# Kernel optimization log

Hardware: AMD Instinct MI355X
Metric: run time of the kernel (lower is better)

Reference implementation:

```python
import jax, jax.numpy as jnp
import numpy as np

NUM_SEM, MAXPP, FS, FG, H, ITERS, ETN, GROUPS = 24, 10, 128, 128, 128, 2, 4, 16
N_NODES, N_EDGES = 20000, 320000


def _leaky(x):
    return jax.nn.leaky_relu(x, 0.01)


def _lin_init(k, din, dout):
    kw, kb = jax.random.split(k)
    lim = 1.0 / np.sqrt(din)
    w = jax.random.uniform(kw, (dout, din), jnp.float32, -lim, lim)
    b = jax.random.uniform(kb, (dout,), jnp.float32, -lim, lim)
    return w, b


def setup_inputs() -> dict:
    key = jax.random.key(0)
    ks = jax.random.split(key, 16)
    inp = {}
    inp["child_feats"] = jax.random.normal(ks[0], (1, N_NODES, NUM_SEM + MAXPP + FS), jnp.float32)
    inp["child_geo_feats"] = jax.random.normal(ks[1], (1, N_NODES, FG), jnp.float32)
    inp["child_exists"] = jnp.ones((1, N_NODES, 1), jnp.float32)
    inp["edge_type_onehot"] = jax.random.uniform(ks[2], (1, N_EDGES, ETN), jnp.float32)
    inp["edge_indices"] = jax.random.randint(ks[3], (1, N_EDGES, 2), 0, N_NODES)
    inp["child_op_w"], inp["child_op_b"] = _lin_init(ks[4], NUM_SEM + MAXPP + FS, H)
    inp["second_w"], inp["second_b"] = _lin_init(ks[5], H * (ITERS + 1), FS)
    ew, eb = zip(*[_lin_init(ks[6 + i], 2 * H + ETN, H) for i in range(ITERS)])
    inp["edge_w"] = jnp.stack(ew)
    inp["edge_b"] = jnp.stack(eb)
    inp["child_geo_w"], inp["child_geo_b"] = _lin_init(ks[10], FG, H)
    inp["second_geo_w"], inp["second_geo_b"] = _lin_init(ks[11], H, FG)
    inp["gn_w"] = jnp.ones((FG,), jnp.float32)
    inp["gn_b"] = jnp.zeros((FG,), jnp.float32)
    inp["skip_w"], inp["skip_b"] = _lin_init(ks[12], FG, FG)
    return inp


def _group_norm(x, w, b, groups=GROUPS, eps=1e-5):
    # x: [B, C]  (torch GroupNorm on 2D input)
    B, C = x.shape
    xg = x.reshape(B, groups, C // groups)
    mu = xg.mean(axis=-1, keepdims=True)
    var = xg.var(axis=-1, keepdims=True)
    xn = ((xg - mu) * jax.lax.rsqrt(var + eps)).reshape(B, C)
    return xn * w + b


def reference(child_feats, child_geo_feats, child_exists, edge_type_onehot, edge_indices,
              child_op_w, child_op_b, second_w, second_b, edge_w, edge_b,
              child_geo_w, child_geo_b, second_geo_w, second_geo_b, gn_w, gn_b, skip_w, skip_b):
    B, N, _ = child_feats.shape
    # struct branch
    cf = (child_feats @ child_op_w.T + child_op_b) * child_exists  # [B,N,H]
    iter_parent_feats = [cf.max(axis=1)]                           # symmetric_type='max'
    idx_from = edge_indices[0, :, 0]
    idx_to = edge_indices[0, :, 1]
    ef = edge_type_onehot[0]                                       # [E,ETN]
    for i in range(ITERS):
        # gather endpoints, concat edge type, edge-MLP + leaky relu
        msg = jnp.concatenate([cf[0, idx_from], cf[0, idx_to], ef], axis=1)  # [E,2H+ETN]
        msg = _leaky(msg @ edge_w[i].T + edge_b[i])                          # [E,H]
        # scatter_max into zero-initialized node slots (matches torch_scatter with out=zeros)
        cf = jnp.zeros((N, H), msg.dtype).at[idx_from].max(msg)[None]        # [1,N,H]
        iter_parent_feats.append(cf.max(axis=1))
    parent_feat = _leaky(jnp.concatenate(iter_parent_feats, axis=1) @ second_w.T + second_b)
    # geo branch
    skip = (child_geo_feats @ skip_w.T + skip_b) * child_exists    # [B,N,FG]
    cg = (child_geo_feats @ child_geo_w.T + child_geo_b) * child_exists  # [B,N,H]
    pg = _leaky(cg.max(axis=1))
    sg = _leaky(skip.max(axis=1))
    parent_geo_feat = _leaky(sg + _group_norm(pg @ second_geo_w.T + second_geo_b, gn_w, gn_b))
    return parent_feat, parent_geo_feat
```

## Files before the change

kernel.cpp:

```cpp
#include <hip/hip_runtime.h>

#define N_NODES 20000
#define N_EDGES 320000
#define HD 128
#define FIN 162
#define KE 260
#define KPAD 288
#define KOP 192
#define WSTR 296
#define OSTR 200
#define GSTR 136
#define TSTR 136
#define RSTR 260

typedef unsigned short u16;
typedef __attribute__((ext_vector_type(8))) short bf16x8;
typedef __attribute__((ext_vector_type(4))) float f32x4;

__device__ __forceinline__ float leaky(float x){ return fmaxf(x, 0.01f*x); }
__device__ __forceinline__ unsigned fmap(float f){
    unsigned u = __float_as_uint(f);
    return (u & 0x80000000u) ? ~u : (u | 0x80000000u);
}
__device__ __forceinline__ float funmap(unsigned u){
    return __uint_as_float((u & 0x80000000u) ? (u & 0x7fffffffu) : ~u);
}
__device__ __forceinline__ unsigned umax_(unsigned a, unsigned b){ return a > b ? a : b; }
__device__ __forceinline__ u16 f2bf(float x){
    unsigned b = __float_as_uint(x);
    return (u16)((b + 0x7fffu + ((b >> 16) & 1u)) >> 16);
}
__device__ __forceinline__ float bf2f(u16 u){
    return __uint_as_float(((unsigned)u) << 16);
}
__device__ __forceinline__ unsigned cvt_pk_bf16(float lo, float hi){
    unsigned r;
    asm("v_cvt_pk_bf16_f32 %0, %1, %2" : "=v"(r) : "v"(lo), "v"(hi));
    return r;
}

#define PB_W 16
#define PB_F 960
#define PB_G 640
#define PB_H 320
#define PREP_GRID (PB_W + PB_F + PB_G + PB_H)

__global__ __launch_bounds__(256) void prep(
    const float* __restrict__ edge_w, const float* __restrict__ edge_bias,
    u16* __restrict__ Wb,
    const float* __restrict__ op_w,   u16* __restrict__ Wop,
    const float* __restrict__ geo_w,  u16* __restrict__ Wgeo,
    const float* __restrict__ skip_w, u16* __restrict__ Wskip,
    const float* __restrict__ feats,  u16* __restrict__ featsb,
    const float* __restrict__ geof,   u16* __restrict__ geob,
    const int* __restrict__ eidx, int* __restrict__ count)
{
    const int b = blockIdx.x, t = threadIdx.x;
    if (b < PB_W) {
        for (int idx = b * 256 + t; idx < 16384; idx += PB_W * 256) {
            union { u16 us[8]; uint4 v; } pk;
            if (idx < 9216) {
                int layer = idx / 4608, rem = idx - layer * 4608;
                int h = rem / 36, j = rem - h * 36;
                const float* src = edge_w + (size_t)layer * 128 * KE + h * KE;
                #pragma unroll
                for (int kk = 0; kk < 8; ++kk) {
                    int k = j * 8 + kk;
                    pk.us[kk] = (k < KE) ? f2bf(src[k])
                              : (k == 260) ? f2bf(edge_bias[layer * 128 + h])
                              : (u16)0;
                }
                ((uint4*)Wb)[(size_t)layer * 128 * 36 + h * 36 + j] = pk.v;
            } else if (idx < 12288) {
                int rem = idx - 9216;
                int h = rem / 24, j = rem - h * 24;
                const float* src = op_w + h * FIN;
                #pragma unroll
                for (int kk = 0; kk < 8; ++kk) {
                    int k = j * 8 + kk;
                    pk.us[kk] = (k < FIN) ? f2bf(src[k]) : (u16)0;
                }
                ((uint4*)Wop)[h * 24 + j] = pk.v;
            } else {
                int rem = idx - 12288;
                int which = rem >> 11;
                int r2 = rem & 2047;
                const float4* src = (const float4*)((which ? skip_w : geo_w)) + r2 * 2;
                float4 a = src[0], c = src[1];
                pk.us[0]=f2bf(a.x); pk.us[1]=f2bf(a.y); pk.us[2]=f2bf(a.z); pk.us[3]=f2bf(a.w);
                pk.us[4]=f2bf(c.x); pk.us[5]=f2bf(c.y); pk.us[6]=f2bf(c.z); pk.us[7]=f2bf(c.w);
                ((uint4*)(which ? Wskip : Wgeo))[r2] = pk.v;
            }
        }
    } else if (b < PB_W + PB_F) {
        for (int f = (b - PB_W) * 256 + t; f < N_NODES * 24; f += PB_F * 256) {
            int n = f / 24, j = f - n * 24;
            union { u16 us[8]; uint4 v; } pk;
            if (j < 20) {
                const float2* src = (const float2*)(feats + (size_t)n * FIN + j * 8);
                float2 p0 = src[0], p1 = src[1], p2 = src[2], p3 = src[3];
                pk.us[0]=f2bf(p0.x); pk.us[1]=f2bf(p0.y); pk.us[2]=f2bf(p1.x); pk.us[3]=f2bf(p1.y);
                pk.us[4]=f2bf(p2.x); pk.us[5]=f2bf(p2.y); pk.us[6]=f2bf(p3.x); pk.us[7]=f2bf(p3.y);
            } else if (j == 20) {
                float2 p = *(const float2*)(feats + (size_t)n * FIN + 160);
                pk.us[0]=f2bf(p.x); pk.us[1]=f2bf(p.y);
                pk.us[2]=pk.us[3]=pk.us[4]=pk.us[5]=pk.us[6]=pk.us[7]=0;
            } else {
                #pragma unroll
                for (int kk = 0; kk < 8; ++kk) pk.us[kk] = 0;
            }
            ((uint4*)featsb)[(size_t)n * 24 + j] = pk.v;
        }
    } else if (b < PB_W + PB_F + PB_G) {
        for (int g = (b - PB_W - PB_F) * 256 + t; g < N_NODES * 16; g += PB_G * 256) {
            const float4* s = (const float4*)geof + (size_t)g * 2;
            float4 a = s[0], c = s[1];
            union { u16 us[8]; uint4 v; } pk;
            pk.us[0]=f2bf(a.x); pk.us[1]=f2bf(a.y); pk.us[2]=f2bf(a.z); pk.us[3]=f2bf(a.w);
            pk.us[4]=f2bf(c.x); pk.us[5]=f2bf(c.y); pk.us[6]=f2bf(c.z); pk.us[7]=f2bf(c.w);
            ((uint4*)geob)[g] = pk.v;
        }
    } else {
        for (int e = (b - PB_W - PB_F - PB_G) * 256 + t; e < N_EDGES; e += PB_H * 256)
            atomicAdd(&count[eidx[2 * e]], 1);
    }
}

__global__ __launch_bounds__(1024) void scan_offsets(
    const int* __restrict__ count, int* __restrict__ offset)
{
    __shared__ int part[1024];
    const int t = threadIdx.x;
    const int lo = t * 20;
    const int hi = min(lo + 20, N_NODES);
    int s = 0;
    for (int n = lo; n < hi; ++n) s += count[n];
    part[t] = s;
    __syncthreads();
    for (int d = 1; d < 1024; d <<= 1) {
        int v = (t >= d) ? part[t - d] : 0;
        __syncthreads();
        part[t] += v;
        __syncthreads();
    }
    int run = (t > 0) ? part[t - 1] : 0;
    for (int n = lo; n < hi; ++n) { offset[n] = run; run += count[n]; }
}

__global__ __launch_bounds__(256) void mid(
    const int* __restrict__ eidx, const float* __restrict__ ef,
    const int* __restrict__ offset, int* __restrict__ cursor,
    int* __restrict__ from_p, int* __restrict__ to_p, uint2* __restrict__ efb_p,
    const u16* __restrict__ featsb, const u16* __restrict__ geob,
    const float* __restrict__ exists,
    const u16* __restrict__ Wop, const float* __restrict__ op_b,
    const u16* __restrict__ Wgeo, const float* __restrict__ geo_b,
    const u16* __restrict__ Wskip, const float* __restrict__ skip_b,
    u16* __restrict__ cf_a,
    unsigned* __restrict__ ipf0_m, unsigned* __restrict__ pg_m,
    unsigned* __restrict__ sg_m)
{
    __shared__ __align__(16) u16 smem[128 * OSTR];
    __shared__ float ex_s[128];
    __shared__ unsigned colmax_s[128];

    const int blk = blockIdx.x, t = threadIdx.x;
    if (blk < 1250) {
        int e = blk * 256 + t;
        int2 p = ((const int2*)eidx)[e];
        int pos = offset[p.x] + atomicAdd(&cursor[p.x], 1);
        from_p[pos] = p.x; to_p[pos] = p.y;
        float4 e4 = ((const float4*)ef)[e];
        efb_p[pos] = make_uint2(
            (unsigned)f2bf(e4.x) | ((unsigned)f2bf(e4.y) << 16),
            (unsigned)f2bf(e4.z) | ((unsigned)f2bf(e4.w) << 16));
        return;
    }
    const int b = blk - 1250;
    const int mode = (b < 157) ? 0 : (b < 314) ? 1 : 2;
    const int bx = b - (mode == 0 ? 0 : mode == 1 ? 157 : 314);
    const int base = bx * 128;
    const int wave = t >> 6, l = t & 63;
    const int quad = l >> 4, lc = l & 15;
    const int R0 = (wave >> 1) * 64;
    const int C0 = (wave & 1) * 64;

    const u16* W = (mode == 0) ? Wop : (mode == 1) ? Wgeo : Wskip;
    const float* bias = (mode == 0) ? op_b : (mode == 1) ? geo_b : skip_b;
    unsigned* accout = (mode == 0) ? ipf0_m : (mode == 1) ? pg_m : sg_m;
    const int KW = (mode == 0) ? KOP : HD;
    const int SW = (mode == 0) ? OSTR : GSTR;
    const int NCH = (mode == 0) ? 6 : 4;
    const u16* A = (mode == 0) ? featsb : geob;

    {
        const int r = t >> 1, half = t & 1;
        const int nu4 = KW / 16;
        const uint4* src = (const uint4*)(W + (size_t)r * KW) + half * nu4;
        uint4* dst = (uint4*)(smem + r * SW) + half * nu4;
        for (int i = 0; i < nu4; ++i) dst[i] = src[i];
    }
    if (t < 128) {
        int n = base + t; if (n >= N_NODES) n = N_NODES - 1;
        ex_s[t] = exists[n];
        colmax_s[t] = 0u;
    }
    __syncthreads();

    f32x4 acc[4][4];
    #pragma unroll
    for (int i = 0; i < 4; ++i)
        #pragma unroll
        for (int j = 0; j < 4; ++j) acc[i][j] = (f32x4){0.f, 0.f, 0.f, 0.f};

    int nd[4];
    #pragma unroll
    for (int ti = 0; ti < 4; ++ti) {
        int n = base + R0 + ti * 16 + lc;
        nd[ti] = (n < N_NODES) ? n : N_NODES - 1;
    }

    for (int c = 0; c < NCH; ++c) {
        bf16x8 af[4], bfr[4];
        #pragma unroll
        for (int ti = 0; ti < 4; ++ti)
            af[ti] = *(const bf16x8*)(A + (size_t)nd[ti] * KW + c * 32 + quad * 8);
        #pragma unroll
        for (int tj = 0; tj < 4; ++tj)
            bfr[tj] = *(const bf16x8*)(smem + (C0 + tj * 16 + lc) * SW + c * 32 + quad * 8);
        #pragma unroll
        for (int ti = 0; ti < 4; ++ti)
            #pragma unroll
            for (int tj = 0; tj < 4; ++tj)
                acc[ti][tj] = __builtin_amdgcn_mfma_f32_16x16x32_bf16(
                    af[ti], bfr[tj], acc[ti][tj], 0, 0, 0);
    }

    #pragma unroll
    for (int tj = 0; tj < 4; ++tj) {
        const int col = C0 + tj * 16 + lc;
        const float bc = bias[col];
        unsigned mx = 0u;
        #pragma unroll
        for (int ti = 0; ti < 4; ++ti) {
            #pragma unroll
            for (int r = 0; r < 4; ++r) {
                int row = R0 + ti * 16 + quad * 4 + r;
                float x = (acc[ti][tj][r] + bc) * ex_s[row];
                acc[ti][tj][r] = x;
                mx = umax_(mx, fmap(x));
            }
        }
        atomicMax(&colmax_s[col], mx);
    }
    __syncthreads();
    if (t < 128) atomicMax(&accout[t], colmax_s[t]);

    if (mode == 0) {
        #pragma unroll
        for (int ti = 0; ti < 4; ++ti)
            #pragma unroll
            for (int tj = 0; tj < 4; ++tj) {
                const int col = C0 + tj * 16 + lc;
                #pragma unroll
                for (int r = 0; r < 4; ++r)
                    smem[(R0 + ti * 16 + quad * 4 + r) * TSTR + col] = f2bf(acc[ti][tj][r]);
            }
        __syncthreads();
        #pragma unroll
        for (int i = 0; i < 8; ++i) {
            int idx = t + i * 256;
            int row = idx >> 4, c16 = idx & 15;
            int n = base + row;
            if (n < N_NODES) {
                uint4 v = *(const uint4*)(smem + row * TSTR + c16 * 8);
                *(uint4*)(cf_a + (size_t)n * HD + c16 * 8) = v;
            }
        }
    }
}

template<int REDUCE>
__global__ __launch_bounds__(512, 2) void edge_mfma(
    const u16* __restrict__ cfb,
    const int* __restrict__ from_p,
    const int* __restrict__ to_p,
    const uint2* __restrict__ efb_p,
    const u16* __restrict__ Wb,
    const int* __restrict__ offs,
    const int* __restrict__ cnt,
    u16* __restrict__ cf_bb,
    float* __restrict__ cf_b32,
    int* __restrict__ ipf_out)
{
    __shared__ __align__(16) u16 smem[128 * WSTR];
    __shared__ int colmax_s[128];

    const int t    = threadIdx.x;
    const int base = blockIdx.x * 512;
    const int wave = t >> 6, l = t & 63;
    const int quad = l >> 4, lc = l & 15;
    const int R0 = wave * 64;

    for (int idx = t; idx < 128 * 36; idx += 512) {
        int r = idx / 36, j = idx - r * 36;
        ((uint4*)(smem + r * WSTR))[j] = ((const uint4*)(Wb + (size_t)r * KPAD))[j];
    }
    if (t < 128) colmax_s[t] = 0;

    int nf[4], nt[4]; uint2 efr[4];
    #pragma unroll
    for (int ti = 0; ti < 4; ++ti) {
        int e = base + R0 + ti * 16 + lc;
        nf[ti]  = from_p[e];
        nt[ti]  = to_p[e];
        efr[ti] = efb_p[e];
    }
    __syncthreads();

    f32x4 acc[4][8];
    #pragma unroll
    for (int i = 0; i < 4; ++i)
        #pragma unroll
        for (int j = 0; j < 8; ++j) acc[i][j] = (f32x4){0.f, 0.f, 0.f, 0.f};

    #pragma unroll
    for (int c = 0; c < 8; ++c) {
        bf16x8 af[4], bfr[8];
        #pragma unroll
        for (int ti = 0; ti < 4; ++ti) {
            int node = (c < 4) ? nf[ti] : nt[ti];
            af[ti] = *(const bf16x8*)(cfb + node * HD + (c & 3) * 32 + quad * 8);
        }
        #pragma unroll
        for (int tj = 0; tj < 8; ++tj)
            bfr[tj] = *(const bf16x8*)(smem + (tj * 16 + lc) * WSTR + c * 32 + quad * 8);
        #pragma unroll
        for (int ti = 0; ti < 4; ++ti)
            #pragma unroll
            for (int tj = 0; tj < 8; ++tj)
                acc[ti][tj] = __builtin_amdgcn_mfma_f32_16x16x32_bf16(
                    af[ti], bfr[tj], acc[ti][tj], 0, 0, 0);
    }
    {
        bf16x8 af[4], bfr[8];
        #pragma unroll
        for (int ti = 0; ti < 4; ++ti) {
            union { bf16x8 v; unsigned u[4]; } p;
            p.u[0] = efr[ti].x; p.u[1] = efr[ti].y;
            p.u[2] = 0x00003f80u;
            p.u[3] = 0u;
            union { bf16x8 v; unsigned u[4]; } z;
            z.u[0] = z.u[1] = z.u[2] = z.u[3] = 0u;
            af[ti] = (quad == 0) ? p.v : z.v;
        }
        #pragma unroll
        for (int tj = 0; tj < 8; ++tj)
            bfr[tj] = *(const bf16x8*)(smem + (tj * 16 + lc) * WSTR + 8 * 32 + quad * 8);
        #pragma unroll
        for (int ti = 0; ti < 4; ++ti)
            #pragma unroll
            for (int tj = 0; tj < 8; ++tj)
                acc[ti][tj] = __builtin_amdgcn_mfma_f32_16x16x32_bf16(
                    af[ti], bfr[tj], acc[ti][tj], 0, 0, 0);
    }

    #pragma unroll
    for (int tj = 0; tj < 8; ++tj) {
        const int cl = tj * 16 + lc;
        float mx = 0.f;
        #pragma unroll
        for (int ti = 0; ti < 4; ++ti) {
            #pragma unroll
            for (int r = 0; r < 4; ++r) {
                float x = leaky(acc[ti][tj][r]);
                acc[ti][tj][r] = x;
                mx = fmaxf(mx, x);
            }
        }
        atomicMax(&colmax_s[cl], __float_as_int(mx));
    }
    __syncthreads();
    if (t < 128) atomicMax(&ipf_out[t], colmax_s[t]);

    if (REDUCE) {
        const int ch  = t & 127;
        const int grp = t >> 7;
        #pragma unroll
        for (int ph = 0; ph < 2; ++ph) {
            if ((R0 >> 8) == ph) {
                const int rb = R0 & 255;
                #pragma unroll
                for (int ti = 0; ti < 4; ++ti)
                    #pragma unroll
                    for (int tj = 0; tj < 8; ++tj) {
                        const int cl = tj * 16 + lc;
                        const int rowb = rb + ti * 16 + quad * 4;
                        uint2 pk;
                        pk.x = cvt_pk_bf16(acc[ti][tj][0], acc[ti][tj][1]);
                        pk.y = cvt_pk_bf16(acc[ti][tj][2], acc[ti][tj][3]);
                        *(uint2*)(smem + cl * RSTR + rowb) = pk;
                    }
            }
            __syncthreads();
            const int wb = base + ph * 256;
            const int nfirst = from_p[wb];
            const int nlast  = from_p[wb + 255];
            for (int n = nfirst + grp; n <= nlast; n += 4) {
                int o = offs[n], c = cnt[n];
                int lo = o - wb, hi = o + c - wb;
                int lo2 = lo > 0 ? lo : 0;
                int hi2 = hi < 256 ? hi : 256;
                if (lo2 >= hi2) continue;
                float m = 0.f;
                for (int r = lo2; r < hi2; ++r)
                    m = fmaxf(m, bf2f(smem[ch * RSTR + r]));
                if (lo >= 0 && hi <= 256)
                    cf_bb[(size_t)n * HD + ch] = f2bf(m);
                else
                    atomicMax((int*)&cf_b32[(size_t)n * HD + ch], __float_as_int(m));
            }
            __syncthreads();
        }
    }
}

__global__ __launch_bounds__(256) void fixup(
    const int* __restrict__ offs, const int* __restrict__ cnt,
    const float* __restrict__ cf_b32, u16* __restrict__ cf_bb)
{
    const int n = blockIdx.x * 2 + (threadIdx.x >> 7);
    const int ch = threadIdx.x & 127;
    int o = offs[n], c = cnt[n];
    if (c > 0 && (o >> 8) != ((o + c - 1) >> 8))
        cf_bb[(size_t)n * HD + ch] = f2bf(cf_b32[(size_t)n * HD + ch]);
}

__global__ __launch_bounds__(128) void heads(
    const unsigned* __restrict__ ipf0_m,
    const float* __restrict__ ipf1, const float* __restrict__ ipf2,
    const float* __restrict__ secW, const float* __restrict__ secB,
    const unsigned* __restrict__ pg_m, const unsigned* __restrict__ sg_m,
    const float* __restrict__ geoW, const float* __restrict__ geoB,
    const float* __restrict__ gnw, const float* __restrict__ gnb,
    float* __restrict__ out)
{
    const int t = threadIdx.x;
    if (blockIdx.x == 0) {
        __shared__ float s[384];
        s[t]       = funmap(ipf0_m[t]);
        s[128 + t] = ipf1[t];
        s[256 + t] = ipf2[t];
        __syncthreads();
        float acc = secB[t];
        #pragma unroll 4
        for (int k = 0; k < 384; ++k) acc = fmaf(s[k], secW[t*384 + k], acc);
        out[t] = leaky(acc);
    } else {
        __shared__ float pg[128];
        __shared__ float tt[128];
        pg[t] = leaky(funmap(pg_m[t]));
        float sg = leaky(funmap(sg_m[t]));
        __syncthreads();
        float acc = geoB[t];
        #pragma unroll 4
        for (int k = 0; k < 128; ++k) acc = fmaf(pg[k], geoW[t*128 + k], acc);
        tt[t] = acc;
        __syncthreads();
        const int g = (t >> 3) << 3;
        float mu = 0.f, m2 = 0.f;
        #pragma unroll
        for (int q = 0; q < 8; ++q) { float x = tt[g + q]; mu += x; m2 += x*x; }
        mu *= 0.125f;
        m2 = m2 * 0.125f - mu * mu;
        float xn = (acc - mu) * rsqrtf(m2 + 1e-5f);
        out[128 + t] = leaky(sg + xn * gnw[t] + gnb[t]);
    }
}

extern "C" void kernel_launch(void* const* d_in, const int* in_sizes, int n_in,
                              void* d_out, int out_size, void* d_ws, size_t ws_size,
                              hipStream_t stream)
{
    const float* child_feats  = (const float*)d_in[0];
    const float* child_geo    = (const float*)d_in[1];
    const float* child_exists = (const float*)d_in[2];
    const float* etoh         = (const float*)d_in[3];
    const int*   eidx         = (const int*)  d_in[4];
    const float* op_w   = (const float*)d_in[5];
    const float* op_b   = (const float*)d_in[6];
    const float* sec_w  = (const float*)d_in[7];
    const float* sec_b  = (const float*)d_in[8];
    const float* edge_w = (const float*)d_in[9];
    const float* edge_b = (const float*)d_in[10];
    const float* geo_w  = (const float*)d_in[11];
    const float* geo_b  = (const float*)d_in[12];
    const float* sgeo_w = (const float*)d_in[13];
    const float* sgeo_b = (const float*)d_in[14];
    const float* gn_w   = (const float*)d_in[15];
    const float* gn_b   = (const float*)d_in[16];
    const float* skip_w = (const float*)d_in[17];
    const float* skip_b = (const float*)d_in[18];
    float* out = (float*)d_out;

    char* ws = (char*)d_ws;
    size_t off = 0;
    u16*   cf_a   = (u16*)(ws + off);   off += (size_t)N_NODES*HD*2;
    u16*   featsb = (u16*)(ws + off);   off += (size_t)N_NODES*KOP*2;
    u16*   geob   = (u16*)(ws + off);   off += (size_t)N_NODES*HD*2;
    u16*   Wb     = (u16*)(ws + off);   off += (size_t)2*128*KPAD*2;
    u16*   Wop    = (u16*)(ws + off);   off += (size_t)128*KOP*2;
    u16*   Wgeo   = (u16*)(ws + off);   off += (size_t)128*128*2;
    u16*   Wskip  = (u16*)(ws + off);   off += (size_t)128*128*2;
    int*   from_p = (int*)(ws + off);   off += (size_t)N_EDGES*4;
    int*   to_p   = (int*)(ws + off);   off += (size_t)N_EDGES*4;
    uint2* efb_p  = (uint2*)(ws + off); off += (size_t)N_EDGES*8;
    int*   offs   = (int*)(ws + off);   off += (size_t)N_NODES*4;
    char*  zero0  = ws + off;
    u16*   cf_bb  = (u16*)(ws + off);         off += (size_t)N_NODES*HD*2;
    float* cf_b32 = (float*)(ws + off);       off += (size_t)N_NODES*HD*4;
    unsigned* ipf0_m = (unsigned*)(ws + off); off += 128*4;
    float*    ipf1   = (float*)(ws + off);    off += 128*4;
    float*    ipf2   = (float*)(ws + off);    off += 128*4;
    unsigned* pg_m   = (unsigned*)(ws + off); off += 128*4;
    unsigned* sg_m   = (unsigned*)(ws + off); off += 128*4;
    int*      count  = (int*)(ws + off);      off += (size_t)N_NODES*4;
    int*      cursor = (int*)(ws + off);      off += (size_t)N_NODES*4;
    size_t zero_bytes = (size_t)(ws + off - zero0);

    hipMemsetAsync(zero0, 0, zero_bytes, stream);

    prep<<<PREP_GRID, 256, 0, stream>>>(
        edge_w, edge_b, Wb, op_w, Wop, geo_w, Wgeo, skip_w, Wskip,
        child_feats, featsb, child_geo, geob, eidx, count);

    scan_offsets<<<1, 1024, 0, stream>>>(count, offs);

    mid<<<1721, 256, 0, stream>>>(
        eidx, etoh, offs, cursor, from_p, to_p, efb_p,
        featsb, geob, child_exists, Wop, op_b, Wgeo, geo_b, Wskip, skip_b,
        cf_a, ipf0_m, pg_m, sg_m);

    edge_mfma<1><<<N_EDGES/512, 512, 0, stream>>>(
        cf_a, from_p, to_p, efb_p, Wb,
        offs, count, cf_bb, cf_b32, (int*)ipf1);

    fixup<<<N_NODES/2, 256, 0, stream>>>(offs, count, cf_b32, cf_bb);

    edge_mfma<0><<<N_EDGES/512, 512, 0, stream>>>(
        cf_bb, from_p, to_p, efb_p, Wb + 128*KPAD,
        offs, count, nullptr, nullptr, (int*)ipf2);

    heads<<<2, 128, 0, stream>>>(ipf0_m, ipf1, ipf2, sec_w, sec_b,
                                 pg_m, sg_m, sgeo_w, sgeo_b, gn_w, gn_b, out);
}
```

Before: 307.5 us.

## Factor edge MLP into per-node GEMM plus per-edge gather-add with segmented max

The edge linear layer is split algebraically: W·[cf_from; cf_to; ef] becomes a per-node GEMM producing both the from-half and to-half projections (with bias), followed by a per-edge pass that adds the gathered to-projection and a small 4-term edge-type dot product. The new pass assigns one wavefront per source node and walks its CSR segment to take the max, so the separate reduce/fixup kernels and the from_p array are no longer needed. This replaces the E×260×128 per-edge MFMA work with N×128×256 node work plus per-edge fp32 gathers of 128 floats. The risk is higher gather bandwidth from the fp32 Y buffer and load imbalance from degree skew across wavefronts.

```diff
diff --git a/kernel.cpp b/kernel.cpp
--- a/kernel.cpp
+++ b/kernel.cpp
@@ -7,11 +7,10 @@
 #define KE 260
 #define KPAD 288
 #define KOP 192
-#define WSTR 296
 #define OSTR 200
 #define GSTR 136
 #define TSTR 136
-#define RSTR 260
+#define YSTR 136
 
 typedef unsigned short u16;
 typedef __attribute__((ext_vector_type(8))) short bf16x8;
@@ -150,7 +149,7 @@
 __global__ __launch_bounds__(256) void mid(
     const int* __restrict__ eidx, const float* __restrict__ ef,
     const int* __restrict__ offset, int* __restrict__ cursor,
-    int* __restrict__ from_p, int* __restrict__ to_p, uint2* __restrict__ efb_p,
+    int* __restrict__ to_p, uint2* __restrict__ efb_p,
     const u16* __restrict__ featsb, const u16* __restrict__ geob,
     const float* __restrict__ exists,
     const u16* __restrict__ Wop, const float* __restrict__ op_b,
@@ -169,7 +168,7 @@
         int e = blk * 256 + t;
         int2 p = ((const int2*)eidx)[e];
         int pos = offset[p.x] + atomicAdd(&cursor[p.x], 1);
-        from_p[pos] = p.x; to_p[pos] = p.y;
+        to_p[pos] = p.y;
         float4 e4 = ((const float4*)ef)[e];
         efb_p[pos] = make_uint2(
             (unsigned)f2bf(e4.x) | ((unsigned)f2bf(e4.y) << 16),
@@ -280,160 +279,145 @@
     }
 }
 
-template<int REDUCE>
-__global__ __launch_bounds__(512, 2) void edge_mfma(
-    const u16* __restrict__ cfb,
-    const int* __restrict__ from_p,
+__global__ __launch_bounds__(512) void ygemm(
+    const u16* __restrict__ cf,
+    const u16* __restrict__ Wb_l,
+    const float* __restrict__ eb,
+    float* __restrict__ Y)
+{
+    __shared__ __align__(16) u16 smem[256 * YSTR];
+    const int t = threadIdx.x;
+    const int base = blockIdx.x * 128;
+    const int wave = t >> 6, l = t & 63;
+    const int quad = l >> 4, lc = l & 15;
+    const int R0 = (wave >> 2) * 64;
+    const int C0 = (wave & 3) * 64;
+
+    for (int idx = t; idx < 4096; idx += 512) {
+        int r = idx >> 4, j = idx & 15;
+        const uint4* src = (const uint4*)(Wb_l +
+            (size_t)((r < 128) ? r * KPAD : (r - 128) * KPAD + 128));
+        ((uint4*)(smem + r * YSTR))[j] = src[j];
+    }
+    __syncthreads();
+
+    f32x4 acc[4][4];
+    #pragma unroll
+    for (int i = 0; i < 4; ++i)
+        #pragma unroll
+        for (int j = 0; j < 4; ++j) acc[i][j] = (f32x4){0.f, 0.f, 0.f, 0.f};
+
+    int nd[4];
+    #pragma unroll
+    for (int ti = 0; ti < 4; ++ti) {
+        int n = base + R0 + ti * 16 + lc;
+        nd[ti] = (n < N_NODES) ? n : N_NODES - 1;
+    }
+
+    #pragma unroll
+    for (int c = 0; c < 4; ++c) {
+        bf16x8 af[4], bfr[4];
+        #pragma unroll
+        for (int ti = 0; ti < 4; ++ti)
+            af[ti] = *(const bf16x8*)(cf + (size_t)nd[ti] * HD + c * 32 + quad * 8);
+        #pragma unroll
+        for (int tj = 0; tj < 4; ++tj)
+            bfr[tj] = *(const bf16x8*)(smem + (C0 + tj * 16 + lc) * YSTR + c * 32 + quad * 8);
+        #pragma unroll
+        for (int ti = 0; ti < 4; ++ti)
+            #pragma unroll
+            for (int tj = 0; tj < 4; ++tj)
+                acc[ti][tj] = __builtin_amdgcn_mfma_f32_16x16x32_bf16(
+                    af[ti], bfr[tj], acc[ti][tj], 0, 0, 0);
+    }
+
+    #pragma unroll
+    for (int tj = 0; tj < 4; ++tj) {
+        const int col = C0 + tj * 16 + lc;
+        const float bc = (col >= 128) ? eb[col - 128] : 0.f;
+        #pragma unroll
+        for (int ti = 0; ti < 4; ++ti) {
+            #pragma unroll
+            for (int r = 0; r < 4; ++r) {
+                int row = base + R0 + ti * 16 + quad * 4 + r;
+                if (row < N_NODES)
+                    Y[(size_t)row * 256 + col] = acc[ti][tj][r] + bc;
+            }
+        }
+    }
+}
+
+template<int WRITE_CF>
+__global__ __launch_bounds__(512) void epass(
+    const float* __restrict__ Y,
     const int* __restrict__ to_p,
     const uint2* __restrict__ efb_p,
-    const u16* __restrict__ Wb,
+    const u16* __restrict__ Wb_l,
     const int* __restrict__ offs,
     const int* __restrict__ cnt,
     u16* __restrict__ cf_bb,
-    float* __restrict__ cf_b32,
     int* __restrict__ ipf_out)
 {
-    __shared__ __align__(16) u16 smem[128 * WSTR];
-    __shared__ int colmax_s[128];
-
-    const int t    = threadIdx.x;
-    const int base = blockIdx.x * 512;
-    const int wave = t >> 6, l = t & 63;
-    const int quad = l >> 4, lc = l & 15;
-    const int R0 = wave * 64;
-
-    for (int idx = t; idx < 128 * 36; idx += 512) {
-        int r = idx / 36, j = idx - r * 36;
-        ((uint4*)(smem + r * WSTR))[j] = ((const uint4*)(Wb + (size_t)r * KPAD))[j];
-    }
-    if (t < 128) colmax_s[t] = 0;
-
-    int nf[4], nt[4]; uint2 efr[4];
-    #pragma unroll
-    for (int ti = 0; ti < 4; ++ti) {
-        int e = base + R0 + ti * 16 + lc;
-        nf[ti]  = from_p[e];
-        nt[ti]  = to_p[e];
-        efr[ti] = efb_p[e];
-    }
+    __shared__ int ipf_s[128];
+    const int t = threadIdx.x;
+    const int l = t & 63;
+    const int n = blockIdx.x * 8 + (t >> 6);
+    if (t < 128) ipf_s[t] = 0;
     __syncthreads();
 
-    f32x4 acc[4][8];
-    #pragma unroll
-    for (int i = 0; i < 4; ++i)
-        #pragma unroll
-        for (int j = 0; j < 8; ++j) acc[i][j] = (f32x4){0.f, 0.f, 0.f, 0.f};
-
-    #pragma unroll
-    for (int c = 0; c < 8; ++c) {
-        bf16x8 af[4], bfr[8];
-        #pragma unroll
-        for (int ti = 0; ti < 4; ++ti) {
-            int node = (c < 4) ? nf[ti] : nt[ti];
-            af[ti] = *(const bf16x8*)(cfb + node * HD + (c & 3) * 32 + quad * 8);
-        }
-        #pragma unroll
-        for (int tj = 0; tj < 8; ++tj)
-            bfr[tj] = *(const bf16x8*)(smem + (tj * 16 + lc) * WSTR + c * 32 + quad * 8);
-        #pragma unroll
-        for (int ti = 0; ti < 4; ++ti)
-            #pragma unroll
-            for (int tj = 0; tj < 8; ++tj)
-                acc[ti][tj] = __builtin_amdgcn_mfma_f32_16x16x32_bf16(
-                    af[ti], bfr[tj], acc[ti][tj], 0, 0, 0);
-    }
-    {
-        bf16x8 af[4], bfr[8];
-        #pragma unroll
-        for (int ti = 0; ti < 4; ++ti) {
-            union { bf16x8 v; unsigned u[4]; } p;
-            p.u[0] = efr[ti].x; p.u[1] = efr[ti].y;
-            p.u[2] = 0x00003f80u;
-            p.u[3] = 0u;
-            union { bf16x8 v; unsigned u[4]; } z;
-            z.u[0] = z.u[1] = z.u[2] = z.u[3] = 0u;
-            af[ti] = (quad == 0) ? p.v : z.v;
-        }
-        #pragma unroll
-        for (int tj = 0; tj < 8; ++tj)
-            bfr[tj] = *(const bf16x8*)(smem + (tj * 16 + lc) * WSTR + 8 * 32 + quad * 8);
-        #pragma unroll
-        for (int ti = 0; ti < 4; ++ti)
-            #pragma unroll
-            for (int tj = 0; tj < 8; ++tj)
-                acc[ti][tj] = __builtin_amdgcn_mfma_f32_16x16x32_bf16(
-                    af[ti], bfr[tj], acc[ti][tj], 0, 0, 0);
-    }
-
-    #pragma unroll
-    for (int tj = 0; tj < 8; ++tj) {
-        const int cl = tj * 16 + lc;
-        float mx = 0.f;
-        #pragma unroll
-        for (int ti = 0; ti < 4; ++ti) {
-            #pragma unroll
-            for (int r = 0; r < 4; ++r) {
-                float x = leaky(acc[ti][tj][r]);
-                acc[ti][tj][r] = x;
-                mx = fmaxf(mx, x);
-            }
-        }
-        atomicMax(&colmax_s[cl], __float_as_int(mx));
-    }
+    const int o = offs[n], c = cnt[n];
+    const float2 yf = *(const float2*)(Y + (size_t)n * 256 + 2 * l);
+    const uint2 wua = *(const uint2*)(Wb_l + (size_t)(2 * l) * KPAD + 256);
+    const uint2 wub = *(const uint2*)(Wb_l + (size_t)(2 * l + 1) * KPAD + 256);
+    const float wa0 = bf2f((u16)wua.x), wa1 = bf2f((u16)(wua.x >> 16));
+    const float wa2 = bf2f((u16)wua.y), wa3 = bf2f((u16)(wua.y >> 16));
+    const float wb0 = bf2f((u16)wub.x), wb1 = bf2f((u16)(wub.x >> 16));
+    const float wb2 = bf2f((u16)wub.y), wb3 = bf2f((u16)(wub.y >> 16));
+
+    float mx0 = 0.f, mx1 = 0.f;
+
+#define EPROC(F, YV) do { \
+    float e0 = bf2f((u16)((F).x)), e1 = bf2f((u16)((F).x >> 16)); \
+    float e2 = bf2f((u16)((F).y)), e3 = bf2f((u16)((F).y >> 16)); \
+    float s0 = yf.x + (YV).x; \
+    s0 = fmaf(e0, wa0, s0); s0 = fmaf(e1, wa1, s0); \
+    s0 = fmaf(e2, wa2, s0); s0 = fmaf(e3, wa3, s0); \
+    s0 = leaky(s0); mx0 = fmaxf(mx0, s0); \
+    float s1 = yf.y + (YV).y; \
+    s1 = fmaf(e0, wb0, s1); s1 = fmaf(e1, wb1, s1); \
+    s1 = fmaf(e2, wb2, s1); s1 = fmaf(e3, wb3, s1); \
+    s1 = leaky(s1); mx1 = fmaxf(mx1, s1); \
+} while (0)
+
+    int i = 0;
+    for (; i + 4 <= c; i += 4) {
+        const int e = o + i;
+        int n0 = to_p[e], n1 = to_p[e + 1], n2 = to_p[e + 2], n3 = to_p[e + 3];
+        uint2 f0 = efb_p[e],     f1 = efb_p[e + 1];
+        uint2 f2 = efb_p[e + 2], f3 = efb_p[e + 3];
+        float2 y0 = *(const float2*)(Y + (size_t)n0 * 256 + 128 + 2 * l);
+        float2 y1 = *(const float2*)(Y + (size_t)n1 * 256 + 128 + 2 * l);
+        float2 y2 = *(const float2*)(Y + (size_t)n2 * 256 + 128 + 2 * l);
+        float2 y3 = *(const float2*)(Y + (size_t)n3 * 256 + 128 + 2 * l);
+        EPROC(f0, y0); EPROC(f1, y1); EPROC(f2, y2); EPROC(f3, y3);
+    }
+    for (; i < c; ++i) {
+        const int e = o + i;
+        int n0 = to_p[e];
+        uint2 f0 = efb_p[e];
+        float2 y0 = *(const float2*)(Y + (size_t)n0 * 256 + 128 + 2 * l);
+        EPROC(f0, y0);
+    }
+#undef EPROC
+
+    if (WRITE_CF) {
+        unsigned pk = cvt_pk_bf16(mx0, mx1);
+        *(unsigned*)(cf_bb + (size_t)n * HD + 2 * l) = pk;
+    }
+    atomicMax(&ipf_s[2 * l],     __float_as_int(mx0));
+    atomicMax(&ipf_s[2 * l + 1], __float_as_int(mx1));
     __syncthreads();
-    if (t < 128) atomicMax(&ipf_out[t], colmax_s[t]);
-
-    if (REDUCE) {
-        const int ch  = t & 127;
-        const int grp = t >> 7;
-        #pragma unroll
-        for (int ph = 0; ph < 2; ++ph) {
-            if ((R0 >> 8) == ph) {
-                const int rb = R0 & 255;
-                #pragma unroll
-                for (int ti = 0; ti < 4; ++ti)
-                    #pragma unroll
-                    for (int tj = 0; tj < 8; ++tj) {
-                        const int cl = tj * 16 + lc;
-                        const int rowb = rb + ti * 16 + quad * 4;
-                        uint2 pk;
-                        pk.x = cvt_pk_bf16(acc[ti][tj][0], acc[ti][tj][1]);
-                        pk.y = cvt_pk_bf16(acc[ti][tj][2], acc[ti][tj][3]);
-                        *(uint2*)(smem + cl * RSTR + rowb) = pk;
-                    }
-            }
-            __syncthreads();
-            const int wb = base + ph * 256;
-            const int nfirst = from_p[wb];
-            const int nlast  = from_p[wb + 255];
-            for (int n = nfirst + grp; n <= nlast; n += 4) {
-                int o = offs[n], c = cnt[n];
-                int lo = o - wb, hi = o + c - wb;
-                int lo2 = lo > 0 ? lo : 0;
-                int hi2 = hi < 256 ? hi : 256;
-                if (lo2 >= hi2) continue;
-                float m = 0.f;
-                for (int r = lo2; r < hi2; ++r)
-                    m = fmaxf(m, bf2f(smem[ch * RSTR + r]));
-                if (lo >= 0 && hi <= 256)
-                    cf_bb[(size_t)n * HD + ch] = f2bf(m);
-                else
-                    atomicMax((int*)&cf_b32[(size_t)n * HD + ch], __float_as_int(m));
-            }
-            __syncthreads();
-        }
-    }
-}
-
-__global__ __launch_bounds__(256) void fixup(
-    const int* __restrict__ offs, const int* __restrict__ cnt,
-    const float* __restrict__ cf_b32, u16* __restrict__ cf_bb)
-{
-    const int n = blockIdx.x * 2 + (threadIdx.x >> 7);
-    const int ch = threadIdx.x & 127;
-    int o = offs[n], c = cnt[n];
-    if (c > 0 && (o >> 8) != ((o + c - 1) >> 8))
-        cf_bb[(size_t)n * HD + ch] = f2bf(cf_b32[(size_t)n * HD + ch]);
+    if (t < 128) atomicMax(&ipf_out[t], ipf_s[t]);
 }
 
 __global__ __launch_bounds__(128) void heads(
@@ -506,19 +490,19 @@
     char* ws = (char*)d_ws;
     size_t off = 0;
     u16*   cf_a   = (u16*)(ws + off);   off += (size_t)N_NODES*HD*2;
-    u16*   featsb = (u16*)(ws + off);   off += (size_t)N_NODES*KOP*2;
-    u16*   geob   = (u16*)(ws + off);   off += (size_t)N_NODES*HD*2;
+    char*  uni    = ws + off;           off += (size_t)N_NODES*256*4;
+    u16*   featsb = (u16*)uni;
+    u16*   geob   = (u16*)(uni + (size_t)N_NODES*KOP*2);
+    float* Y      = (float*)uni;
     u16*   Wb     = (u16*)(ws + off);   off += (size_t)2*128*KPAD*2;
     u16*   Wop    = (u16*)(ws + off);   off += (size_t)128*KOP*2;
     u16*   Wgeo   = (u16*)(ws + off);   off += (size_t)128*128*2;
     u16*   Wskip  = (u16*)(ws + off);   off += (size_t)128*128*2;
-    int*   from_p = (int*)(ws + off);   off += (size_t)N_EDGES*4;
     int*   to_p   = (int*)(ws + off);   off += (size_t)N_EDGES*4;
     uint2* efb_p  = (uint2*)(ws + off); off += (size_t)N_EDGES*8;
     int*   offs   = (int*)(ws + off);   off += (size_t)N_NODES*4;
     char*  zero0  = ws + off;
     u16*   cf_bb  = (u16*)(ws + off);         off += (size_t)N_NODES*HD*2;
-    float* cf_b32 = (float*)(ws + off);       off += (size_t)N_NODES*HD*4;
     unsigned* ipf0_m = (unsigned*)(ws + off); off += 128*4;
     float*    ipf1   = (float*)(ws + off);    off += 128*4;
     float*    ipf2   = (float*)(ws + off);    off += 128*4;
@@ -537,19 +521,17 @@
     scan_offsets<<<1, 1024, 0, stream>>>(count, offs);
 
     mid<<<1721, 256, 0, stream>>>(
-        eidx, etoh, offs, cursor, from_p, to_p, efb_p,
+        eidx, etoh, offs, cursor, to_p, efb_p,
         featsb, geob, child_exists, Wop, op_b, Wgeo, geo_b, Wskip, skip_b,
         cf_a, ipf0_m, pg_m, sg_m);
 
-    edge_mfma<1><<<N_EDGES/512, 512, 0, stream>>>(
-        cf_a, from_p, to_p, efb_p, Wb,
-        offs, count, cf_bb, cf_b32, (int*)ipf1);
-
-    fixup<<<N_NODES/2, 256, 0, stream>>>(offs, count, cf_b32, cf_bb);
-
-    edge_mfma<0><<<N_EDGES/512, 512, 0, stream>>>(
-        cf_bb, from_p, to_p, efb_p, Wb + 128*KPAD,
-        offs, count, nullptr, nullptr, (int*)ipf2);
+    ygemm<<<157, 512, 0, stream>>>(cf_a, Wb, edge_b, Y);
+    epass<1><<<N_NODES/8, 512, 0, stream>>>(
+        Y, to_p, efb_p, Wb, offs, count, cf_bb, (int*)ipf1);
+
+    ygemm<<<157, 512, 0, stream>>>(cf_bb, Wb + 128*KPAD, edge_b + 128, Y);
+    epass<0><<<N_NODES/8, 512, 0, stream>>>(
+        Y, to_p, efb_p, Wb + 128*KPAD, offs, count, nullptr, (int*)ipf2);
 
     heads<<<2, 128, 0, stream>>>(ipf0_m, ipf1, ipf2, sec_w, sec_b,
                                  pg_m, sg_m, sgeo_w, sgeo_b, gn_w, gn_b, out);
```

Result: slower. 340.7 us (+10.8%).
